# Optimization experiments

Hardware: AMD Instinct MI355X
Metric: run time of the kernel (lower is better)

## Reference

```python
import jax, jax.numpy as jnp
import numpy as np

D_MODEL = 1024
N_HEADS = 16
D_HEAD = D_MODEL // N_HEADS
LATENT = 64
B, T = 2, 2048


def setup_inputs() -> dict:
    key = jax.random.key(0)
    ks = jax.random.split(key, 6)
    s = lambda fan_in: 1.0 / np.sqrt(fan_in)
    return {
        "x": jax.random.normal(ks[0], (B, T, D_MODEL), dtype=jnp.float32),
        "w_c": jax.random.normal(ks[1], (D_MODEL, LATENT), dtype=jnp.float32) * s(D_MODEL),
        "w_k": jax.random.normal(ks[2], (LATENT, D_MODEL), dtype=jnp.float32) * s(LATENT),
        "w_v": jax.random.normal(ks[3], (LATENT, D_MODEL), dtype=jnp.float32) * s(LATENT),
        "w_q": jax.random.normal(ks[4], (D_MODEL, D_MODEL), dtype=jnp.float32) * s(D_MODEL),
        "w_o": jax.random.normal(ks[5], (D_MODEL, D_MODEL), dtype=jnp.float32) * s(D_MODEL),
    }


def _split_heads(t):
    # [B, T, D] -> [B, H, T, d_head]
    b, tt, _ = t.shape
    return t.reshape(b, tt, N_HEADS, D_HEAD).transpose(0, 2, 1, 3)


def reference(x, w_c, w_k, w_v, w_q, w_o):
    latent = x @ w_c                      # [B, T, L] low-rank KV compression
    K = _split_heads(latent @ w_k)        # [B, H, T, d]
    V = _split_heads(latent @ w_v)
    Q = _split_heads(x @ w_q)
    scale = 1.0 / jnp.sqrt(jnp.float32(D_HEAD))
    scores = jnp.einsum("bhqd,bhkd->bhqk", Q, K) * scale
    tq = x.shape[1]
    causal = jnp.tril(jnp.ones((tq, tq), dtype=jnp.float32))
    scores = scores + (1.0 - causal) * -1e9  # additive mask, matching original
    attn = jax.nn.softmax(scores, axis=-1)
    out = jnp.einsum("bhqk,bhkd->bhqd", attn, V)
    out = out.transpose(0, 2, 1, 3).reshape(x.shape[0], tq, D_MODEL)
    return out @ w_o
```

## Files before the change

### kernel.cpp

```cpp
#include <hip/hip_runtime.h>
#include <hip/hip_bf16.h>
#include <cstdint>
#include <cstddef>

typedef __bf16 bf16;
typedef __attribute__((ext_vector_type(8))) __bf16 bf16x8;
typedef __attribute__((ext_vector_type(4))) __bf16 bf16x4;
typedef __attribute__((ext_vector_type(4))) float f32x4;
typedef __attribute__((ext_vector_type(16))) float f32x16;
typedef __attribute__((ext_vector_type(4))) unsigned int u32x4;

#define MFMA16x16x32(a, b, c) __builtin_amdgcn_mfma_f32_16x16x32_bf16((a), (b), (c), 0, 0, 0)
#define MFMA32x32x16(a, b, c) __builtin_amdgcn_mfma_f32_32x32x16_bf16((a), (b), (c), 0, 0, 0)

__device__ __forceinline__ void gload16(const void* g, void* l) {
  __builtin_amdgcn_global_load_lds((const __attribute__((address_space(1))) unsigned int*)g,
                                   (__attribute__((address_space(3))) unsigned int*)l,
                                   16, 0, 0);
}

__device__ __forceinline__ unsigned packbf(float a, float b) {
  unsigned short ua = __builtin_bit_cast(unsigned short, (bf16)a);
  unsigned short ub = __builtin_bit_cast(unsigned short, (bf16)b);
  return (unsigned)ua | ((unsigned)ub << 16);
}

__device__ __forceinline__ float fexp2(float x) {
  float r;
  asm("v_exp_f32 %0, %1" : "=v"(r) : "v"(x));
  return r;
}

__global__ __launch_bounds__(256) void prep_fused(const float* __restrict__ x,
                                                  const float* __restrict__ w_c,
                                                  const float* __restrict__ w_k,
                                                  const float* __restrict__ w_v,
                                                  const float* __restrict__ w_q,
                                                  const float* __restrict__ w_o,
                                                  bf16* __restrict__ xb,
                                                  bf16* __restrict__ BTq,
                                                  bf16* __restrict__ WoutT) {
  __shared__ __align__(16) char smem[2 * 64 * 65 * 4];
  const int bi = blockIdx.x;
  const int t = threadIdx.x;

  if (bi < 4096) {
    int i = bi * 256 + t;
    float4 v = reinterpret_cast<const float4*>(x)[i];
    bf16x4 o;
    o[0] = (bf16)v.x; o[1] = (bf16)v.y; o[2] = (bf16)v.z; o[3] = (bf16)v.w;
    *reinterpret_cast<bf16x4*>(xb + (size_t)i * 4) = o;
    return;
  }

  if (bi < 4112) {
    auto tile = (bf16(*)[72])smem;
    const int r0 = (bi - 4096) * 64;
    bf16* out = BTq + (size_t)1024 * 1024;
    {
      int rr = t >> 4;
      int cc = (t & 15) * 4;
#pragma unroll
      for (int p = 0; p < 4; ++p) {
        float4 v = *(const float4*)&w_c[(size_t)(r0 + rr + 16 * p) * 64 + cc];
        bf16x4 o;
        o[0] = (bf16)v.x; o[1] = (bf16)v.y; o[2] = (bf16)v.z; o[3] = (bf16)v.w;
        *(bf16x4*)&tile[rr + 16 * p][cc] = o;
      }
    }
    __syncthreads();
    {
      int cc = t >> 3;
      int rr = (t & 7) * 8;
#pragma unroll
      for (int p = 0; p < 2; ++p) {
        bf16x8 v;
#pragma unroll
        for (int j = 0; j < 8; ++j) v[j] = tile[rr + j][cc + 32 * p];
        *(bf16x8*)&out[(size_t)(cc + 32 * p) * 1024 + r0 + rr] = v;
      }
    }
    return;
  }

  auto Aq = (float(*)[65])smem;
  auto Ak = (float(*)[65])(smem + 64 * 65 * 4);

  if (bi < 4368) {
    const int blk = bi - 4112;
    const int h = blk >> 4, dm0 = (blk & 15) * 64;
    {
      int row = t >> 2, c0 = (t & 3) * 16;
#pragma unroll
      for (int j = 0; j < 4; ++j) {
        float4 vq = *(const float4*)&w_q[(size_t)(dm0 + row) * 1024 + h * 64 + c0 + 4 * j];
        Aq[row][c0 + 4 * j + 0] = vq.x; Aq[row][c0 + 4 * j + 1] = vq.y;
        Aq[row][c0 + 4 * j + 2] = vq.z; Aq[row][c0 + 4 * j + 3] = vq.w;
        float4 vk = *(const float4*)&w_k[(size_t)row * 1024 + h * 64 + c0 + 4 * j];
        Ak[row][c0 + 4 * j + 0] = vk.x; Ak[row][c0 + 4 * j + 1] = vk.y;
        Ak[row][c0 + 4 * j + 2] = vk.z; Ak[row][c0 + 4 * j + 3] = vk.w;
      }
    }
    __syncthreads();
    const int ld0 = (t >> 4) * 4, dmq = (t & 15) * 4;
    float acc[4][4] = {};
    for (int dh = 0; dh < 64; ++dh) {
      float rk[4], rq[4];
#pragma unroll
      for (int i = 0; i < 4; ++i) rk[i] = Ak[ld0 + i][dh];
#pragma unroll
      for (int j = 0; j < 4; ++j) rq[j] = Aq[dmq + j][dh];
#pragma unroll
      for (int i = 0; i < 4; ++i)
#pragma unroll
        for (int j = 0; j < 4; ++j) acc[i][j] += rk[i] * rq[j];
    }
    const float S = 0.18033688011112042f;
#pragma unroll
    for (int i = 0; i < 4; ++i) {
      bf16x4 o;
#pragma unroll
      for (int j = 0; j < 4; ++j) o[j] = (bf16)(acc[i][j] * S);
      *(bf16x4*)&BTq[(size_t)(h * 64 + ld0 + i) * 1024 + dm0 + dmq] = o;
    }
    return;
  }

  {
    const int blk = bi - 4368;
    const int h = blk >> 4, dn0 = (blk & 15) * 64;
    {
      int row = t >> 2, c0 = (t & 3) * 16;
#pragma unroll
      for (int j = 0; j < 4; ++j) {
        float4 vv = *(const float4*)&w_v[(size_t)row * 1024 + h * 64 + c0 + 4 * j];
        Aq[row][c0 + 4 * j + 0] = vv.x; Aq[row][c0 + 4 * j + 1] = vv.y;
        Aq[row][c0 + 4 * j + 2] = vv.z; Aq[row][c0 + 4 * j + 3] = vv.w;
        float4 vo = *(const float4*)&w_o[(size_t)(h * 64 + row) * 1024 + dn0 + c0 + 4 * j];
        Ak[row][c0 + 4 * j + 0] = vo.x; Ak[row][c0 + 4 * j + 1] = vo.y;
        Ak[row][c0 + 4 * j + 2] = vo.z; Ak[row][c0 + 4 * j + 3] = vo.w;
      }
    }
    __syncthreads();
    const int dnq = (t >> 4) * 4, lv0 = (t & 15) * 4;
    float acc[4][4] = {};
    for (int dh = 0; dh < 64; ++dh) {
      float ro[4], rv[4];
#pragma unroll
      for (int i = 0; i < 4; ++i) ro[i] = Ak[dh][dnq + i];
#pragma unroll
      for (int j = 0; j < 4; ++j) rv[j] = Aq[lv0 + j][dh];
#pragma unroll
      for (int i = 0; i < 4; ++i)
#pragma unroll
        for (int j = 0; j < 4; ++j) acc[i][j] += ro[i] * rv[j];
    }
#pragma unroll
    for (int i = 0; i < 4; ++i) {
      bf16x4 o;
#pragma unroll
      for (int j = 0; j < 4; ++j) o[j] = (bf16)acc[i][j];
      *(bf16x4*)&WoutT[(size_t)(dn0 + dnq + i) * 1024 + h * 64 + lv0] = o;
    }
  }
}

__global__ __launch_bounds__(256) void make_latT(const bf16* __restrict__ QL,
                                                 bf16* __restrict__ latT) {
  __shared__ __align__(16) bf16 tile[64][72];
  const int r0 = blockIdx.x * 64;
  const int t = threadIdx.x;
  {
    int row = t >> 2, c0 = (t & 3) * 16;
    const bf16* src = QL + (size_t)(r0 + row) * 1088 + 1024 + c0;
    *(bf16x8*)&tile[row][c0] = *(const bf16x8*)src;
    *(bf16x8*)&tile[row][c0 + 8] = *(const bf16x8*)(src + 8);
  }
  __syncthreads();
  {
    int d = t >> 2, tc = (t & 3) * 16;
    const int g1[8] = {0, 1, 2, 3, 8, 9, 10, 11};
    const int g2[8] = {4, 5, 6, 7, 12, 13, 14, 15};
    bf16x8 v0, v1;
#pragma unroll
    for (int j = 0; j < 8; ++j) {
      v0[j] = tile[tc + g1[j]][d];
      v1[j] = tile[tc + g2[j]][d];
    }
    *(bf16x8*)&latT[(size_t)d * 4096 + r0 + tc] = v0;
    *(bf16x8*)&latT[(size_t)d * 4096 + r0 + tc + 8] = v1;
  }
}

template <int BM, int BN, int WM, int WN, bool OUT_F32>
__global__ __launch_bounds__(256) void gemm_bf16(const bf16* __restrict__ A,
                                                 const bf16* __restrict__ BT,
                                                 void* __restrict__ C,
                                                 int N, int K) {
  constexpr int BK = 32;
  constexpr int TM = (BM / WM) / 16;
  constexpr int TN = (BN / WN) / 16;
  __shared__ __align__(16) bf16 As[BM * BK];
  __shared__ __align__(16) bf16 Bs[BN * BK];
  const int tid = threadIdx.x;
  const int lane = tid & 63;
  const int wid = tid >> 6;
  const int wm = wid / WN;
  const int wn = wid % WN;
  const int bm = blockIdx.x * BM;
  const int bn = blockIdx.y * BN;
  const int arow = lane & 15;
  const int koff = (lane >> 4) * 8;

  f32x4 acc[TM][TN] = {};

  for (int kb = 0; kb < K; kb += BK) {
    for (int base = wid * 1024; base < BM * 64; base += 4096) {
      int off = base + lane * 16;
      int row = off >> 6;
      int col = off & 63;
      gload16((const char*)A + ((size_t)(bm + row) * K + kb) * 2 + col, (char*)As + base);
    }
    for (int base = wid * 1024; base < BN * 64; base += 4096) {
      int off = base + lane * 16;
      int row = off >> 6;
      int col = off & 63;
      gload16((const char*)BT + ((size_t)(bn + row) * K + kb) * 2 + col, (char*)Bs + base);
    }
    __syncthreads();

    bf16x8 af[TM], bfr[TN];
#pragma unroll
    for (int i = 0; i < TM; ++i)
      af[i] = *(const bf16x8*)&As[(wm * TM * 16 + i * 16 + arow) * BK + koff];
#pragma unroll
    for (int j = 0; j < TN; ++j)
      bfr[j] = *(const bf16x8*)&Bs[(wn * TN * 16 + j * 16 + arow) * BK + koff];
#pragma unroll
    for (int i = 0; i < TM; ++i)
#pragma unroll
      for (int j = 0; j < TN; ++j)
        acc[i][j] = MFMA16x16x32(af[i], bfr[j], acc[i][j]);
    __syncthreads();
  }

  const int m0 = bm + wm * TM * 16 + (lane >> 4) * 4;
  const int n0 = bn + wn * TN * 16 + (lane & 15);
#pragma unroll
  for (int i = 0; i < TM; ++i)
#pragma unroll
    for (int j = 0; j < TN; ++j)
#pragma unroll
      for (int r = 0; r < 4; ++r) {
        int m = m0 + i * 16 + r;
        int n = n0 + j * 16;
        float v = acc[i][j][r];
        if constexpr (OUT_F32)
          ((float*)C)[(size_t)m * N + n] = v;
        else
          ((bf16*)C)[(size_t)m * N + n] = (bf16)v;
      }
}

__global__ __launch_bounds__(256) void mla_attn5(const bf16* __restrict__ QL,
                                                 const bf16* __restrict__ latT,
                                                 bf16* __restrict__ out_lat) {
  __shared__ __align__(16) bf16 Kst[2][2048];
  __shared__ __align__(16) bf16 Vst[2][2048];
  __shared__ __align__(16) bf16 etile[4][32][72];
  const int tid = threadIdx.x, lane = tid & 63, w = tid >> 6;
  const int c_raw = blockIdx.x & 63;
  const int rest = (int)(blockIdx.x >> 6);
  const int b = rest & 1;
  const int hg = (rest >> 1) & 3;
  const int c = (rest < 4) ? (63 - c_raw) : c_raw;
  const int h = hg * 4 + w;
  const int nt = c + 1;
  const int q0 = c * 32;
  const int li = lane & 31;
  const int hb = lane >> 5;
  const size_t boff = (size_t)b * 2048;
  const bf16* lat = QL + 1024;

  const int drow = tid >> 3;
  const int dbyte = (tid & 7) * 16;
  const int sbyte = dbyte ^ ((drow & 7) << 4);
  const int vd = 2 * drow + (sbyte >> 6);
  const int vkof = (sbyte & 63) >> 1;
  auto stage = [&](int buf, int kb) {
    gload16((const char*)lat + ((size_t)(boff + kb + drow) * 1088) * 2 + sbyte,
            (char*)&Kst[buf][0] + w * 1024);
    gload16((const char*)latT + ((size_t)vd * 4096 + boff + kb + vkof) * 2,
            (char*)&Vst[buf][0] + w * 1024);
  };

  bf16x8 qf[4];
  {
    const bf16* qp = QL + ((size_t)(boff + q0 + li)) * 1088 + h * 64 + hb * 8;
#pragma unroll
    for (int s = 0; s < 4; ++s) qf[s] = *(const bf16x8*)(qp + 16 * s);
  }

  float lsum = 0.f;
  f32x16 ot0 = {}, ot1 = {};

  stage(0, 0);
  for (int t = 0; t < nt; ++t) {
    const int cur = t & 1;
    if (t + 1 < nt) {
      stage(cur ^ 1, (t + 1) * 32);
      asm volatile("s_waitcnt vmcnt(2)" ::: "memory");
    } else {
      asm volatile("s_waitcnt vmcnt(0)" ::: "memory");
    }
    __builtin_amdgcn_s_barrier();
    __builtin_amdgcn_sched_barrier(0);

    bf16x8 ka[4], va[2][2];
#pragma unroll
    for (int s = 0; s < 4; ++s)
      ka[s] = *(const bf16x8*)((const char*)&Kst[cur][0] + li * 128 +
                               ((hb * 16 + 32 * s) ^ ((li & 7) << 4)));
#pragma unroll
    for (int ldb = 0; ldb < 2; ++ldb) {
      const int srow = 16 * ldb + (li >> 1);
#pragma unroll
      for (int s2 = 0; s2 < 2; ++s2) {
        const int vb = (li & 1) * 64 + hb * 16 + 32 * s2;
        va[ldb][s2] = *(const bf16x8*)((const char*)&Vst[cur][0] + srow * 128 +
                                       (vb ^ ((srow & 7) << 4)));
      }
    }

    f32x16 st = {};
    __builtin_amdgcn_s_setprio(1);
#pragma unroll
    for (int s = 0; s < 4; ++s) st = MFMA32x32x16(ka[s], qf[s], st);
    __builtin_amdgcn_s_setprio(0);
    if (t == nt - 1) {
#pragma unroll
      for (int r = 0; r < 16; ++r) {
        const int krow = (r & 3) + 8 * (r >> 2) + 4 * hb;
        if (krow > li) st[r] = -30000.f;
      }
    }
    float pv[16];
#pragma unroll
    for (int r = 0; r < 16; ++r) {
      pv[r] = fexp2(st[r]);
      lsum += pv[r];
    }
    u32x4 w1, w2;
    w1[0] = packbf(pv[0], pv[1]);  w1[1] = packbf(pv[2], pv[3]);
    w1[2] = packbf(pv[4], pv[5]);  w1[3] = packbf(pv[6], pv[7]);
    w2[0] = packbf(pv[8], pv[9]);  w2[1] = packbf(pv[10], pv[11]);
    w2[2] = packbf(pv[12], pv[13]); w2[3] = packbf(pv[14], pv[15]);
    const bf16x8 pb1 = __builtin_bit_cast(bf16x8, w1);
    const bf16x8 pb2 = __builtin_bit_cast(bf16x8, w2);
    __builtin_amdgcn_s_setprio(1);
    ot0 = MFMA32x32x16(va[0][0], pb1, ot0);
    ot0 = MFMA32x32x16(va[0][1], pb2, ot0);
    ot1 = MFMA32x32x16(va[1][0], pb1, ot1);
    ot1 = MFMA32x32x16(va[1][1], pb2, ot1);
    __builtin_amdgcn_s_setprio(0);

    __builtin_amdgcn_sched_barrier(0);
    asm volatile("s_waitcnt lgkmcnt(0)" ::: "memory");
    __builtin_amdgcn_s_barrier();
  }

  lsum += __shfl_xor(lsum, 32);

  const float inv = 1.0f / lsum;
#pragma unroll
  for (int r = 0; r < 16; ++r) {
    const int ldr = (r & 3) + 8 * (r >> 2) + 4 * hb;
    etile[w][li][ldr] = (bf16)(ot0[r] * inv);
    etile[w][li][ldr + 32] = (bf16)(ot1[r] * inv);
  }
  asm volatile("s_waitcnt lgkmcnt(0)" ::: "memory");
  __builtin_amdgcn_sched_barrier(0);
  {
    bf16* op = out_lat + ((size_t)(boff + q0 + li)) * 1024 + h * 64 + hb * 32;
#pragma unroll
    for (int j = 0; j < 4; ++j)
      *(bf16x8*)(op + 8 * j) = *(const bf16x8*)&etile[w][li][hb * 32 + 8 * j];
  }
}

extern "C" void kernel_launch(void* const* d_in, const int* in_sizes, int n_in,
                              void* d_out, int out_size, void* d_ws, size_t ws_size,
                              hipStream_t stream) {
  const float* x   = (const float*)d_in[0];
  const float* w_c = (const float*)d_in[1];
  const float* w_k = (const float*)d_in[2];
  const float* w_v = (const float*)d_in[3];
  const float* w_q = (const float*)d_in[4];
  const float* w_o = (const float*)d_in[5];
  float* out = (float*)d_out;

  char* ws = (char*)d_ws;
  size_t off = 0;
  auto alloc = [&](size_t bytes) {
    char* p = ws + off;
    off += (bytes + 255) & ~(size_t)255;
    return p;
  };
  bf16* xb     = (bf16*)alloc((size_t)4096 * 1024 * 2);
  bf16* QLbuf  = (bf16*)alloc((size_t)4096 * 1088 * 2);
  bf16* BTq    = (bf16*)alloc((size_t)1088 * 1024 * 2);
  bf16* latT   = (bf16*)alloc((size_t)64 * 4096 * 2);
  bf16* outlat = (bf16*)alloc((size_t)4096 * 1024 * 2);
  bf16* WoutT  = (bf16*)alloc((size_t)1024 * 1024 * 2);

  prep_fused<<<4624, 256, 0, stream>>>(x, w_c, w_k, w_v, w_q, w_o, xb, BTq, WoutT);

  gemm_bf16<128, 64, 2, 2, false><<<dim3(32, 17), 256, 0, stream>>>(
      xb, BTq, QLbuf, 1088, 1024);

  make_latT<<<64, 256, 0, stream>>>(QLbuf, latT);

  mla_attn5<<<512, 256, 0, stream>>>(QLbuf, latT, outlat);

  gemm_bf16<64, 128, 1, 4, true><<<dim3(64, 8), 256, 0, stream>>>(
      outlat, WoutT, (void*)out, 1024, 1024);

  (void)in_sizes; (void)n_in; (void)out_size; (void)ws_size;
}
```

Baseline: 124.3 us.

## Deepen attention K/V staging to four buffers and double GEMM K-tile

The attention kernel moves from double-buffered to a four-slot ring of K/V stages with a prefetch distance of two. This lets it drop the trailing barrier at the end of each iteration, since a slot is not overwritten until two iterations later. The GEMM kernel gains a BK template parameter set to 64, which halves the number of K-loop iterations and barriers while doubling shared memory per block. The costs are more LDS per block, which may lower occupancy, and reliance on the distance-2 ring for correctness now that the end-of-iteration sync is gone.

```diff
diff --git a/kernel.cpp b/kernel.cpp
--- a/kernel.cpp
+++ b/kernel.cpp
@@ -192,14 +192,15 @@
   }
 }
 
-template <int BM, int BN, int WM, int WN, bool OUT_F32>
+template <int BM, int BN, int BK, int WM, int WN, bool OUT_F32>
 __global__ __launch_bounds__(256) void gemm_bf16(const bf16* __restrict__ A,
                                                  const bf16* __restrict__ BT,
                                                  void* __restrict__ C,
                                                  int N, int K) {
-  constexpr int BK = 32;
   constexpr int TM = (BM / WM) / 16;
   constexpr int TN = (BN / WN) / 16;
+  constexpr int KK = BK / 32;
+  constexpr int ROWB = BK * 2;
   __shared__ __align__(16) bf16 As[BM * BK];
   __shared__ __align__(16) bf16 Bs[BN * BK];
   const int tid = threadIdx.x;
@@ -215,32 +216,38 @@
   f32x4 acc[TM][TN] = {};
 
   for (int kb = 0; kb < K; kb += BK) {
-    for (int base = wid * 1024; base < BM * 64; base += 4096) {
+    for (int base = wid * 1024; base < BM * ROWB; base += 4096) {
       int off = base + lane * 16;
-      int row = off >> 6;
-      int col = off & 63;
+      int row = off / ROWB;
+      int col = off % ROWB;
       gload16((const char*)A + ((size_t)(bm + row) * K + kb) * 2 + col, (char*)As + base);
     }
-    for (int base = wid * 1024; base < BN * 64; base += 4096) {
+    for (int base = wid * 1024; base < BN * ROWB; base += 4096) {
       int off = base + lane * 16;
-      int row = off >> 6;
-      int col = off & 63;
+      int row = off / ROWB;
+      int col = off % ROWB;
       gload16((const char*)BT + ((size_t)(bn + row) * K + kb) * 2 + col, (char*)Bs + base);
     }
     __syncthreads();
 
-    bf16x8 af[TM], bfr[TN];
+    bf16x8 af[TM][KK], bfr[TN][KK];
 #pragma unroll
     for (int i = 0; i < TM; ++i)
-      af[i] = *(const bf16x8*)&As[(wm * TM * 16 + i * 16 + arow) * BK + koff];
+#pragma unroll
+      for (int kk = 0; kk < KK; ++kk)
+        af[i][kk] = *(const bf16x8*)&As[(wm * TM * 16 + i * 16 + arow) * BK + kk * 32 + koff];
 #pragma unroll
     for (int j = 0; j < TN; ++j)
-      bfr[j] = *(const bf16x8*)&Bs[(wn * TN * 16 + j * 16 + arow) * BK + koff];
+#pragma unroll
+      for (int kk = 0; kk < KK; ++kk)
+        bfr[j][kk] = *(const bf16x8*)&Bs[(wn * TN * 16 + j * 16 + arow) * BK + kk * 32 + koff];
 #pragma unroll
     for (int i = 0; i < TM; ++i)
 #pragma unroll
       for (int j = 0; j < TN; ++j)
-        acc[i][j] = MFMA16x16x32(af[i], bfr[j], acc[i][j]);
+#pragma unroll
+        for (int kk = 0; kk < KK; ++kk)
+          acc[i][j] = MFMA16x16x32(af[i][kk], bfr[j][kk], acc[i][j]);
     __syncthreads();
   }
 
@@ -265,8 +272,8 @@
 __global__ __launch_bounds__(256) void mla_attn5(const bf16* __restrict__ QL,
                                                  const bf16* __restrict__ latT,
                                                  bf16* __restrict__ out_lat) {
-  __shared__ __align__(16) bf16 Kst[2][2048];
-  __shared__ __align__(16) bf16 Vst[2][2048];
+  __shared__ __align__(16) bf16 Kst[4][2048];
+  __shared__ __align__(16) bf16 Vst[4][2048];
   __shared__ __align__(16) bf16 etile[4][32][72];
   const int tid = threadIdx.x, lane = tid & 63, w = tid >> 6;
   const int c_raw = blockIdx.x & 63;
@@ -305,10 +312,13 @@
   f32x16 ot0 = {}, ot1 = {};
 
   stage(0, 0);
+  if (nt > 1) stage(1, 32);
   for (int t = 0; t < nt; ++t) {
-    const int cur = t & 1;
-    if (t + 1 < nt) {
-      stage(cur ^ 1, (t + 1) * 32);
+    const int cur = t & 3;
+    if (t + 2 < nt) {
+      stage((t + 2) & 3, (t + 2) * 32);
+      asm volatile("s_waitcnt vmcnt(4)" ::: "memory");
+    } else if (t + 1 < nt) {
       asm volatile("s_waitcnt vmcnt(2)" ::: "memory");
     } else {
       asm volatile("s_waitcnt vmcnt(0)" ::: "memory");
@@ -363,10 +373,6 @@
     ot1 = MFMA32x32x16(va[1][0], pb1, ot1);
     ot1 = MFMA32x32x16(va[1][1], pb2, ot1);
     __builtin_amdgcn_s_setprio(0);
-
-    __builtin_amdgcn_sched_barrier(0);
-    asm volatile("s_waitcnt lgkmcnt(0)" ::: "memory");
-    __builtin_amdgcn_s_barrier();
   }
 
   lsum += __shfl_xor(lsum, 32);
@@ -415,14 +421,14 @@
 
   prep_fused<<<4624, 256, 0, stream>>>(x, w_c, w_k, w_v, w_q, w_o, xb, BTq, WoutT);
 
-  gemm_bf16<128, 64, 2, 2, false><<<dim3(32, 17), 256, 0, stream>>>(
+  gemm_bf16<128, 64, 64, 2, 2, false><<<dim3(32, 17), 256, 0, stream>>>(
       xb, BTq, QLbuf, 1088, 1024);
 
   make_latT<<<64, 256, 0, stream>>>(QLbuf, latT);
 
   mla_attn5<<<512, 256, 0, stream>>>(QLbuf, latT, outlat);
 
-  gemm_bf16<64, 128, 1, 4, true><<<dim3(64, 8), 256, 0, stream>>>(
+  gemm_bf16<64, 128, 64, 1, 4, true><<<dim3(64, 8), 256, 0, stream>>>(
       outlat, WoutT, (void*)out, 1024, 1024);
 
   (void)in_sizes; (void)n_in; (void)out_size; (void)ws_size;
```

New measurement: 127.0 us. 1.02x slower.

## Triple-buffer GEMM and attention staging and process 64-key tiles

Applied to the files above, without the earlier changes.

The GEMM kernel moves from single-buffered LDS loads with two __syncthreads per k-step to a three-stage async global-to-LDS pipeline with one barrier per step. The attention kernel now handles 64 keys per iteration, so it runs half as many barrier-separated steps, and it uses a three-deep staging buffer with the trailing barrier and lgkmcnt wait removed. The V staging layout is changed to read latT rows directly, and the causal mask is applied only to the relevant half. The cost is more LDS per block, which may lower occupancy, and the removed trailing barrier relies on triple buffering to prevent overwriting a buffer still being read.

```diff
diff --git a/kernel.cpp b/kernel.cpp
--- a/kernel.cpp
+++ b/kernel.cpp
@@ -200,8 +200,9 @@
   constexpr int BK = 32;
   constexpr int TM = (BM / WM) / 16;
   constexpr int TN = (BN / WN) / 16;
-  __shared__ __align__(16) bf16 As[BM * BK];
-  __shared__ __align__(16) bf16 Bs[BN * BK];
+  static_assert((BM + BN) * BK * 2 / 4096 == 3, "vmcnt literal assumes 3 loads/thread");
+  __shared__ __align__(16) bf16 As[3][BM * BK];
+  __shared__ __align__(16) bf16 Bs[3][BN * BK];
   const int tid = threadIdx.x;
   const int lane = tid & 63;
   const int wid = tid >> 6;
@@ -212,36 +213,49 @@
   const int arow = lane & 15;
   const int koff = (lane >> 4) * 8;
 
-  f32x4 acc[TM][TN] = {};
-
-  for (int kb = 0; kb < K; kb += BK) {
+  auto stageg = [&](int buf, int kb) {
     for (int base = wid * 1024; base < BM * 64; base += 4096) {
       int off = base + lane * 16;
       int row = off >> 6;
       int col = off & 63;
-      gload16((const char*)A + ((size_t)(bm + row) * K + kb) * 2 + col, (char*)As + base);
+      gload16((const char*)A + ((size_t)(bm + row) * K + kb) * 2 + col,
+              (char*)&As[buf][0] + base);
     }
     for (int base = wid * 1024; base < BN * 64; base += 4096) {
       int off = base + lane * 16;
       int row = off >> 6;
       int col = off & 63;
-      gload16((const char*)BT + ((size_t)(bn + row) * K + kb) * 2 + col, (char*)Bs + base);
-    }
-    __syncthreads();
+      gload16((const char*)BT + ((size_t)(bn + row) * K + kb) * 2 + col,
+              (char*)&Bs[buf][0] + base);
+    }
+  };
+
+  f32x4 acc[TM][TN] = {};
+  const int nkt = K / BK;
+  stageg(0, 0);
+  for (int t = 0; t < nkt; ++t) {
+    const int cur = t % 3;
+    if (t + 1 < nkt) {
+      stageg((t + 1) % 3, (t + 1) * BK);
+      asm volatile("s_waitcnt vmcnt(3)" ::: "memory");
+    } else {
+      asm volatile("s_waitcnt vmcnt(0)" ::: "memory");
+    }
+    __builtin_amdgcn_s_barrier();
+    __builtin_amdgcn_sched_barrier(0);
 
     bf16x8 af[TM], bfr[TN];
 #pragma unroll
     for (int i = 0; i < TM; ++i)
-      af[i] = *(const bf16x8*)&As[(wm * TM * 16 + i * 16 + arow) * BK + koff];
+      af[i] = *(const bf16x8*)&As[cur][(wm * TM * 16 + i * 16 + arow) * BK + koff];
 #pragma unroll
     for (int j = 0; j < TN; ++j)
-      bfr[j] = *(const bf16x8*)&Bs[(wn * TN * 16 + j * 16 + arow) * BK + koff];
+      bfr[j] = *(const bf16x8*)&Bs[cur][(wn * TN * 16 + j * 16 + arow) * BK + koff];
 #pragma unroll
     for (int i = 0; i < TM; ++i)
 #pragma unroll
       for (int j = 0; j < TN; ++j)
         acc[i][j] = MFMA16x16x32(af[i], bfr[j], acc[i][j]);
-    __syncthreads();
   }
 
   const int m0 = bm + wm * TM * 16 + (lane >> 4) * 4;
@@ -262,11 +276,11 @@
       }
 }
 
-__global__ __launch_bounds__(256) void mla_attn5(const bf16* __restrict__ QL,
+__global__ __launch_bounds__(256) void mla_attn6(const bf16* __restrict__ QL,
                                                  const bf16* __restrict__ latT,
                                                  bf16* __restrict__ out_lat) {
-  __shared__ __align__(16) bf16 Kst[2][2048];
-  __shared__ __align__(16) bf16 Vst[2][2048];
+  __shared__ __align__(16) bf16 Kst[3][4096];
+  __shared__ __align__(16) bf16 Vst[3][4096];
   __shared__ __align__(16) bf16 etile[4][32][72];
   const int tid = threadIdx.x, lane = tid & 63, w = tid >> 6;
   const int c_raw = blockIdx.x & 63;
@@ -275,23 +289,31 @@
   const int hg = (rest >> 1) & 3;
   const int c = (rest < 4) ? (63 - c_raw) : c_raw;
   const int h = hg * 4 + w;
-  const int nt = c + 1;
+  const int nt = (c + 2) >> 1;
+  const bool ceven = !(c & 1);
   const int q0 = c * 32;
   const int li = lane & 31;
   const int hb = lane >> 5;
   const size_t boff = (size_t)b * 2048;
   const bf16* lat = QL + 1024;
 
-  const int drow = tid >> 3;
-  const int dbyte = (tid & 7) * 16;
-  const int sbyte = dbyte ^ ((drow & 7) << 4);
-  const int vd = 2 * drow + (sbyte >> 6);
-  const int vkof = (sbyte & 63) >> 1;
+  const int r0i = tid >> 3;
+  const int dby = (tid & 7) * 16;
   auto stage = [&](int buf, int kb) {
-    gload16((const char*)lat + ((size_t)(boff + kb + drow) * 1088) * 2 + sbyte,
-            (char*)&Kst[buf][0] + w * 1024);
-    gload16((const char*)latT + ((size_t)vd * 4096 + boff + kb + vkof) * 2,
-            (char*)&Vst[buf][0] + w * 1024);
+#pragma unroll
+    for (int i = 0; i < 2; ++i) {
+      const int krow = r0i + 32 * i;
+      const int sb = dby ^ ((krow & 7) << 4);
+      gload16((const char*)lat + ((size_t)(boff + kb + krow) * 1088) * 2 + sb,
+              (char*)&Kst[buf][0] + i * 4096 + w * 1024);
+    }
+#pragma unroll
+    for (int i = 0; i < 2; ++i) {
+      const int vrow = r0i + 32 * i;
+      const int sb = dby ^ ((vrow & 7) << 4);
+      gload16((const char*)latT + ((size_t)vrow * 4096 + boff + kb) * 2 + sb,
+              (char*)&Vst[buf][0] + i * 4096 + w * 1024);
+    }
   };
 
   bf16x8 qf[4];
@@ -306,55 +328,76 @@
 
   stage(0, 0);
   for (int t = 0; t < nt; ++t) {
-    const int cur = t & 1;
+    const int cur = t % 3;
     if (t + 1 < nt) {
-      stage(cur ^ 1, (t + 1) * 32);
-      asm volatile("s_waitcnt vmcnt(2)" ::: "memory");
+      stage((t + 1) % 3, (t + 1) * 64);
+      asm volatile("s_waitcnt vmcnt(4)" ::: "memory");
     } else {
       asm volatile("s_waitcnt vmcnt(0)" ::: "memory");
     }
     __builtin_amdgcn_s_barrier();
     __builtin_amdgcn_sched_barrier(0);
 
-    bf16x8 ka[4], va[2][2];
-#pragma unroll
-    for (int s = 0; s < 4; ++s)
-      ka[s] = *(const bf16x8*)((const char*)&Kst[cur][0] + li * 128 +
-                               ((hb * 16 + 32 * s) ^ ((li & 7) << 4)));
+    const bool last = (t == nt - 1);
+    const bool skip1 = last && ceven;
+
+    bf16x8 ka0[4], ka1[4], va[2][4];
+#pragma unroll
+    for (int s = 0; s < 4; ++s) {
+      const int xo = (hb * 16 + 32 * s) ^ ((li & 7) << 4);
+      ka0[s] = *(const bf16x8*)((const char*)&Kst[cur][0] + li * 128 + xo);
+      ka1[s] = *(const bf16x8*)((const char*)&Kst[cur][0] + (32 + li) * 128 + xo);
+    }
 #pragma unroll
     for (int ldb = 0; ldb < 2; ++ldb) {
-      const int srow = 16 * ldb + (li >> 1);
-#pragma unroll
-      for (int s2 = 0; s2 < 2; ++s2) {
-        const int vb = (li & 1) * 64 + hb * 16 + 32 * s2;
-        va[ldb][s2] = *(const bf16x8*)((const char*)&Vst[cur][0] + srow * 128 +
-                                       (vb ^ ((srow & 7) << 4)));
-      }
-    }
-
-    f32x16 st = {};
+      const int vrow = 32 * ldb + li;
+#pragma unroll
+      for (int s2 = 0; s2 < 4; ++s2) {
+        const int vb = (32 * s2 + 16 * hb) ^ ((li & 7) << 4);
+        va[ldb][s2] = *(const bf16x8*)((const char*)&Vst[cur][0] + vrow * 128 + vb);
+      }
+    }
+
+    f32x16 st0 = {}, st1 = {};
     __builtin_amdgcn_s_setprio(1);
 #pragma unroll
-    for (int s = 0; s < 4; ++s) st = MFMA32x32x16(ka[s], qf[s], st);
+    for (int s = 0; s < 4; ++s) st0 = MFMA32x32x16(ka0[s], qf[s], st0);
+    if (!skip1) {
+#pragma unroll
+      for (int s = 0; s < 4; ++s) st1 = MFMA32x32x16(ka1[s], qf[s], st1);
+    }
     __builtin_amdgcn_s_setprio(0);
-    if (t == nt - 1) {
+    if (last) {
 #pragma unroll
       for (int r = 0; r < 16; ++r) {
         const int krow = (r & 3) + 8 * (r >> 2) + 4 * hb;
-        if (krow > li) st[r] = -30000.f;
-      }
-    }
-    float pv[16];
+        if (ceven) {
+          if (krow > li) st0[r] = -30000.f;
+        } else {
+          if (krow > li) st1[r] = -30000.f;
+        }
+      }
+    }
+
+    float pv0[16], pv1[16];
 #pragma unroll
     for (int r = 0; r < 16; ++r) {
-      pv[r] = fexp2(st[r]);
-      lsum += pv[r];
-    }
+      pv0[r] = fexp2(st0[r]);
+      lsum += pv0[r];
+    }
+    if (!skip1) {
+#pragma unroll
+      for (int r = 0; r < 16; ++r) {
+        pv1[r] = fexp2(st1[r]);
+        lsum += pv1[r];
+      }
+    }
+
     u32x4 w1, w2;
-    w1[0] = packbf(pv[0], pv[1]);  w1[1] = packbf(pv[2], pv[3]);
-    w1[2] = packbf(pv[4], pv[5]);  w1[3] = packbf(pv[6], pv[7]);
-    w2[0] = packbf(pv[8], pv[9]);  w2[1] = packbf(pv[10], pv[11]);
-    w2[2] = packbf(pv[12], pv[13]); w2[3] = packbf(pv[14], pv[15]);
+    w1[0] = packbf(pv0[0], pv0[1]);   w1[1] = packbf(pv0[2], pv0[3]);
+    w1[2] = packbf(pv0[4], pv0[5]);   w1[3] = packbf(pv0[6], pv0[7]);
+    w2[0] = packbf(pv0[8], pv0[9]);   w2[1] = packbf(pv0[10], pv0[11]);
+    w2[2] = packbf(pv0[12], pv0[13]); w2[3] = packbf(pv0[14], pv0[15]);
     const bf16x8 pb1 = __builtin_bit_cast(bf16x8, w1);
     const bf16x8 pb2 = __builtin_bit_cast(bf16x8, w2);
     __builtin_amdgcn_s_setprio(1);
@@ -363,10 +406,21 @@
     ot1 = MFMA32x32x16(va[1][0], pb1, ot1);
     ot1 = MFMA32x32x16(va[1][1], pb2, ot1);
     __builtin_amdgcn_s_setprio(0);
-
-    __builtin_amdgcn_sched_barrier(0);
-    asm volatile("s_waitcnt lgkmcnt(0)" ::: "memory");
-    __builtin_amdgcn_s_barrier();
+    if (!skip1) {
+      u32x4 w3, w4;
+      w3[0] = packbf(pv1[0], pv1[1]);   w3[1] = packbf(pv1[2], pv1[3]);
+      w3[2] = packbf(pv1[4], pv1[5]);   w3[3] = packbf(pv1[6], pv1[7]);
+      w4[0] = packbf(pv1[8], pv1[9]);   w4[1] = packbf(pv1[10], pv1[11]);
+      w4[2] = packbf(pv1[12], pv1[13]); w4[3] = packbf(pv1[14], pv1[15]);
+      const bf16x8 pb3 = __builtin_bit_cast(bf16x8, w3);
+      const bf16x8 pb4 = __builtin_bit_cast(bf16x8, w4);
+      __builtin_amdgcn_s_setprio(1);
+      ot0 = MFMA32x32x16(va[0][2], pb3, ot0);
+      ot0 = MFMA32x32x16(va[0][3], pb4, ot0);
+      ot1 = MFMA32x32x16(va[1][2], pb3, ot1);
+      ot1 = MFMA32x32x16(va[1][3], pb4, ot1);
+      __builtin_amdgcn_s_setprio(0);
+    }
   }
 
   lsum += __shfl_xor(lsum, 32);
@@ -420,7 +474,7 @@
 
   make_latT<<<64, 256, 0, stream>>>(QLbuf, latT);
 
-  mla_attn5<<<512, 256, 0, stream>>>(QLbuf, latT, outlat);
+  mla_attn6<<<512, 256, 0, stream>>>(QLbuf, latT, outlat);
 
   gemm_bf16<64, 128, 1, 4, true><<<dim3(64, 8), 256, 0, stream>>>(
       outlat, WoutT, (void*)out, 1024, 1024);
```

Result: faster. 103.8 us (median of 3 runs) (-16.5%).
